# Optimization experiments

Measured on AMD Instinct MI355X. Metric: run time of the kernel, lower is better.

Reference implementation:

```python
import jax, jax.numpy as jnp
import numpy as np

NEG_SLOPE = 0.2  # PyG GATConv default
BN_EPS = 1e-5
NUM_GRAPHS = 128


def _bn(x, g, b, m, v):
    # eval-mode BatchNorm1d with running stats
    return (x - m) * jax.lax.rsqrt(v + BN_EPS) * g + b


def _gat_conv(x, src, dst, mask, W, a_src, a_dst, bias):
    # PyG GATConv: per-head linear, edge logits LeakyReLU(a_src.Wx_j + a_dst.Wx_i),
    # segment-softmax over incoming edges of each dst node, scatter-add messages.
    N = x.shape[0]
    H, C = a_src.shape
    xw = (x @ W).reshape(N, H, C)                       # [N,H,C]
    logit_s = (xw * a_src).sum(-1)                      # [N,H]
    logit_d = (xw * a_dst).sum(-1)                      # [N,H]
    e = jax.nn.leaky_relu(logit_s[src] + logit_d[dst], NEG_SLOPE)  # [E,H]
    e = jnp.where(mask[:, None], e, -1e30)              # edges filtered by edge_weights==1
    m = jax.ops.segment_max(e, dst, num_segments=N)     # [N,H]
    m = jnp.maximum(m, -1e30)                           # guard empty segments
    p = jnp.exp(e - m[dst]) * mask[:, None].astype(e.dtype)
    denom = jax.ops.segment_sum(p, dst, num_segments=N) + 1e-16
    alpha = p / denom[dst]                              # [E,H]
    out = jax.ops.segment_sum(xw[src] * alpha[..., None], dst, num_segments=N)
    return out.reshape(N, H * C) + bias


def setup_inputs() -> dict:
    key = jax.random.key(0)
    ks = jax.random.split(key, 20)
    N, E, F, G, NC = 20000, 320000, 128, NUM_GRAPHS, 10
    E0, E1, H = 256, 512, 2
    C = E1 // H

    def lin(k, fi, fo):
        return jax.random.normal(k, (fi, fo), jnp.float32) / np.float32(np.sqrt(fi))

    def bn(k, n):
        k1, k2, k3, k4 = jax.random.split(k, 4)
        g = 1.0 + 0.1 * jax.random.normal(k1, (n,), jnp.float32)
        b = 0.1 * jax.random.normal(k2, (n,), jnp.float32)
        m = 0.1 * jax.random.normal(k3, (n,), jnp.float32)
        v = 1.0 + 0.5 * jax.random.uniform(k4, (n,), jnp.float32)
        return g, b, m, v

    d = {}
    d['x'] = jax.random.normal(ks[0], (N, F), jnp.float32)
    d['edge_index'] = jax.random.randint(ks[1], (2, E), 0, N, dtype=jnp.int32)
    d['edge_weights'] = jnp.ones((E,), jnp.int32)
    d['batch'] = jnp.sort(jax.random.randint(ks[2], (N,), 0, G, dtype=jnp.int32))
    d['mlp_w1'] = lin(ks[3], F, E0); d['mlp_b1'] = jnp.zeros((E0,), jnp.float32)
    d['bn1_g'], d['bn1_b'], d['bn1_m'], d['bn1_v'] = bn(ks[4], E0)
    d['mlp_w2'] = lin(ks[5], E0, E0); d['mlp_b2'] = jnp.zeros((E0,), jnp.float32)
    d['bn2_g'], d['bn2_b'], d['bn2_m'], d['bn2_v'] = bn(ks[6], E0)
    d['gat0_w'] = lin(ks[7], E0, H * C)
    d['gat0_asrc'] = 0.1 * jax.random.normal(ks[8], (H, C), jnp.float32)
    d['gat0_adst'] = 0.1 * jax.random.normal(ks[9], (H, C), jnp.float32)
    d['gat0_bias'] = jnp.zeros((H * C,), jnp.float32)
    d['gat1_w'] = lin(ks[10], E1, H * C)
    d['gat1_asrc'] = 0.1 * jax.random.normal(ks[11], (H, C), jnp.float32)
    d['gat1_adst'] = 0.1 * jax.random.normal(ks[12], (H, C), jnp.float32)
    d['gat1_bias'] = jnp.zeros((H * C,), jnp.float32)
    d['bn3_g'], d['bn3_b'], d['bn3_m'], d['bn3_v'] = bn(ks[13], E1)
    d['fin_w1'] = lin(ks[14], E1, E1); d['fin_b1'] = jnp.zeros((E1,), jnp.float32)
    d['fin_w2'] = lin(ks[15], E1, NC); d['fin_b2'] = jnp.zeros((NC,), jnp.float32)
    return d


def reference(x, edge_index, edge_weights, batch,
              mlp_w1, mlp_b1, bn1_g, bn1_b, bn1_m, bn1_v,
              mlp_w2, mlp_b2, bn2_g, bn2_b, bn2_m, bn2_v,
              gat0_w, gat0_asrc, gat0_adst, gat0_bias,
              gat1_w, gat1_asrc, gat1_adst, gat1_bias,
              bn3_g, bn3_b, bn3_m, bn3_v,
              fin_w1, fin_b1, fin_w2, fin_b2):
    src, dst = edge_index[0], edge_index[1]
    mask = edge_weights == 1
    # initial MLP (dropout is identity in eval)
    h = jax.nn.relu(_bn(x @ mlp_w1 + mlp_b1, bn1_g, bn1_b, bn1_m, bn1_v))
    h = jax.nn.relu(_bn(h @ mlp_w2 + mlp_b2, bn2_g, bn2_b, bn2_m, bn2_v))
    # GAT layers
    h = _gat_conv(h, src, dst, mask, gat0_w, gat0_asrc, gat0_adst, gat0_bias)
    h = _gat_conv(h, src, dst, mask, gat1_w, gat1_asrc, gat1_adst, gat1_bias)
    # global mean pool over graphs
    sums = jax.ops.segment_sum(h, batch, num_segments=NUM_GRAPHS)
    cnt = jax.ops.segment_sum(jnp.ones((h.shape[0], 1), h.dtype), batch, num_segments=NUM_GRAPHS)
    pooled = sums / jnp.maximum(cnt, 1.0)
    # final head: BN -> ReLU -> Linear -> ReLU -> Linear
    z = jax.nn.relu(_bn(pooled, bn3_g, bn3_b, bn3_m, bn3_v))
    z = jax.nn.relu(z @ fin_w1 + fin_b1)
    return z @ fin_w2 + fin_b2
```

## Files before the change

kernel.cpp:

```cpp
#include <hip/hip_runtime.h>

typedef unsigned short u16;

constexpr int NN = 20000;
constexpr int EE = 320000;
constexpr int FD = 128;
constexpr int C0 = 256;
constexpr int C1 = 512;
constexpr int NG = 128;
constexpr int NC = 10;
constexpr int NBLK = (NN + 255) / 256;
constexpr int HB  = 320;
constexpr int EST = HB * 256;

constexpr size_t OFF_XB   = 0;
constexpr size_t OFF_H1   = OFF_XB  + (size_t)NN * FD * 2;
constexpr size_t OFF_H2   = OFF_H1  + (size_t)NN * C0 * 2;
constexpr size_t OFF_XW   = OFF_H2  + (size_t)NN * C0 * 2;
constexpr size_t OFF_H34  = OFF_XW  + (size_t)NN * C1 * 2;
constexpr size_t OFF_LS   = OFF_H34 + (size_t)NN * C1 * 2;
constexpr size_t OFF_LD   = OFF_LS  + (size_t)NN * 2 * 4;
constexpr size_t OFF_DEG  = OFF_LD  + (size_t)NN * 2 * 4;
constexpr size_t OFF_OFFS = OFF_DEG + (size_t)NN * 4;
constexpr size_t OFF_CUR  = OFF_OFFS + 80016;
constexpr size_t OFF_CSRC = OFF_CUR + (size_t)NN * 4;
constexpr size_t OFF_GCNT = OFF_CSRC + (size_t)EE * 4;
constexpr size_t OFF_GOFF = OFF_GCNT + 512;
constexpr size_t OFF_PART = OFF_GOFF + 768;
constexpr size_t OFF_PTOT = OFF_PART + 512;
constexpr size_t OFF_Z1   = OFF_PTOT + 256;
constexpr size_t OFF_Z2   = OFF_Z1  + (size_t)NG * C1 * 2;
constexpr size_t OFF_ST   = OFF_Z2  + (size_t)NG * C1 * 2;
constexpr size_t OFF_W1T  = OFF_ST  + 8192;
constexpr size_t OFF_W2T  = OFF_W1T + (size_t)FD * C0 * 2;
constexpr size_t OFF_G0T  = OFF_W2T + (size_t)C0 * C0 * 2;
constexpr size_t OFF_G1T  = OFF_G0T + (size_t)C0 * C1 * 2;
constexpr size_t OFF_AUX  = OFF_G1T + (size_t)C1 * C1 * 2;
constexpr size_t OFF_FLAG = OFF_AUX  + 0;
constexpr size_t OFF_A0S  = OFF_AUX  + 256;
constexpr size_t OFF_A0D  = OFF_AUX  + 1280;
constexpr size_t OFF_A1S  = OFF_AUX  + 2304;
constexpr size_t OFF_A1D  = OFF_AUX  + 3328;
constexpr size_t OFF_GB0  = OFF_AUX  + 4352;
constexpr size_t OFF_GB1  = OFF_AUX  + 6400;
constexpr size_t OFF_FB1  = OFF_AUX  + 8448;
constexpr size_t OFF_FB2  = OFF_AUX  + 10496;
constexpr size_t OFF_GMX  = OFF_AUX  + 10752;

__device__ inline float bf2f(u16 u) { return __uint_as_float(((unsigned)u) << 16); }
__device__ inline u16 f2bf(float f) {
    unsigned u = __float_as_uint(f);
    unsigned r = u + 0x7fffu + ((u >> 16) & 1u);
    return (u16)(r >> 16);
}
__device__ inline float ldf(const void* p, long i, unsigned f) {
    return f ? ((const float*)p)[i] : bf2f(((const u16*)p)[i]);
}
__device__ inline unsigned encf(float f) {
    unsigned u = __float_as_uint(f);
    return (u & 0x80000000u) ? ~u : (u | 0x80000000u);
}
__device__ inline float decf(unsigned e) {
    return (e & 0x80000000u) ? __uint_as_float(e ^ 0x80000000u) : __uint_as_float(~e);
}
__device__ inline void unpack8(uint4 r, float* v) {
    v[0] = bf2f((u16)(r.x & 0xffff)); v[1] = bf2f((u16)(r.x >> 16));
    v[2] = bf2f((u16)(r.y & 0xffff)); v[3] = bf2f((u16)(r.y >> 16));
    v[4] = bf2f((u16)(r.z & 0xffff)); v[5] = bf2f((u16)(r.z >> 16));
    v[6] = bf2f((u16)(r.w & 0xffff)); v[7] = bf2f((u16)(r.w >> 16));
}

typedef __bf16 bf16x8_t __attribute__((ext_vector_type(8)));
typedef float  f32x4_t  __attribute__((ext_vector_type(4)));

__device__ __forceinline__ void gl_lds16(const u16* g, u16* l) {
    __builtin_amdgcn_global_load_lds((const __attribute__((address_space(1))) void*)g,
                                     (__attribute__((address_space(3))) void*)l, 16, 0, 0);
}

__global__ void detect_dtype(const u16* __restrict__ x, const u16* __restrict__ w,
                             const u16* __restrict__ fw, unsigned* flag) {
    __shared__ int cnt;
    if (threadIdx.x == 0) cnt = 0;
    __syncthreads();
    int c = 0;
    for (int i = threadIdx.x; i < 4096; i += 256) {
        c += (((x[i]  >> 7) & 0xFF) == 0xFF);
        c += (((w[i]  >> 7) & 0xFF) == 0xFF);
        c += (((fw[i] >> 7) & 0xFF) == 0xFF);
    }
    atomicAdd(&cnt, c);
    __syncthreads();
    if (threadIdx.x == 0) *flag = (cnt >= 2) ? 1u : 0u;
}

__global__ void cvt_x(const unsigned* __restrict__ flag, const void* __restrict__ xin,
                      u16* __restrict__ XB, int* __restrict__ deg, int* __restrict__ gcnt,
                      unsigned* __restrict__ gmxu) {
    int i = blockIdx.x * 256 + threadIdx.x;
    if (i < NN) deg[i] = 0;
    if (i < NG) gcnt[i] = 0;
    if (i < 4)  gmxu[i] = encf(-1e30f);
    if (*flag) {
        float4 v = ((const float4*)xin)[i];
        ushort4 r;
        r.x = f2bf(v.x); r.y = f2bf(v.y); r.z = f2bf(v.z); r.w = f2bf(v.w);
        ((ushort4*)XB)[i] = r;
    } else {
        ((ushort4*)XB)[i] = ((const ushort4*)xin)[i];
    }
}

__global__ void prep_params(const unsigned* __restrict__ flag,
                            const void* g1, const void* b1, const void* m1, const void* v1, const void* lb1,
                            const void* g2, const void* b2, const void* m2, const void* v2, const void* lb2,
                            const void* g3, const void* b3, const void* m3, const void* v3,
                            const void* a0s, const void* a0d, const void* gb0in,
                            const void* a1s, const void* a1d, const void* gb1in,
                            const void* fb1in, const void* fb2in,
                            float* S1, float* T1, float* S2, float* T2, float* S3, float* T3,
                            u16* A0S, u16* A0D, u16* A1S, u16* A1D,
                            float* GB0, float* GB1, float* FB1, float* FB2) {
    unsigned f = *flag;
    int c = threadIdx.x;
    if (c < 256) {
        float s = ldf(g1, c, f) / sqrtf(ldf(v1, c, f) + 1e-5f);
        S1[c] = s; T1[c] = s * (ldf(lb1, c, f) - ldf(m1, c, f)) + ldf(b1, c, f);
        float s2 = ldf(g2, c, f) / sqrtf(ldf(v2, c, f) + 1e-5f);
        S2[c] = s2; T2[c] = s2 * (ldf(lb2, c, f) - ldf(m2, c, f)) + ldf(b2, c, f);
    }
    float s3 = ldf(g3, c, f) / sqrtf(ldf(v3, c, f) + 1e-5f);
    S3[c] = s3; T3[c] = ldf(b3, c, f) - ldf(m3, c, f) * s3;
    A0S[c] = f2bf(ldf(a0s, c, f));
    A0D[c] = f2bf(ldf(a0d, c, f));
    A1S[c] = f2bf(ldf(a1s, c, f));
    A1D[c] = f2bf(ldf(a1d, c, f));
    GB0[c] = ldf(gb0in, c, f);
    GB1[c] = ldf(gb1in, c, f);
    FB1[c] = ldf(fb1in, c, f);
    if (c < NC) FB2[c] = ldf(fb2in, c, f);
}

__global__ void transpose_all(const unsigned* __restrict__ flag,
                              const void* __restrict__ w1, const void* __restrict__ w2,
                              const void* __restrict__ g0, const void* __restrict__ g1,
                              u16* __restrict__ w1T, u16* __restrict__ w2T,
                              u16* __restrict__ g0T, u16* __restrict__ g1T) {
    int b = blockIdx.x;
    const void* B; u16* BT; int K, logN, base;
    if (b < 128)      { B = w1; BT = w1T; K = FD; logN = 8; base = 0; }
    else if (b < 384) { B = w2; BT = w2T; K = C0; logN = 8; base = 128; }
    else if (b < 896) { B = g0; BT = g0T; K = C0; logN = 9; base = 384; }
    else              { B = g1; BT = g1T; K = C1; logN = 9; base = 896; }
    int idx = (b - base) * 256 + threadIdx.x;
    int N = 1 << logN;
    int k = idx >> logN, n = idx & (N - 1);
    u16 v = (*flag) ? f2bf(((const float*)B)[idx]) : ((const u16*)B)[idx];
    BT[(size_t)n * K + k] = v;
}

__global__ __launch_bounds__(256) void hist_k(const int* __restrict__ dst, const int* __restrict__ ew,
                                              const int* __restrict__ batch,
                                              int* __restrict__ deg, int* __restrict__ gcnt) {
    int tid = blockIdx.x * 256 + threadIdx.x;
    int lane = threadIdx.x & 63;
#pragma unroll
    for (int j = 0; j < 4; j++) {
        int e = tid + j * EST;
        if (e < EE && ew[e] == 1) atomicAdd(&deg[dst[e]], 1);
    }
    int n = tid;
    if (n < NN) {
        int g = batch[n];
        int pg = __shfl_up(g, 1);
        bool head = (lane == 0) || (pg != g);
        unsigned long long act = __ballot(1);
        unsigned long long hm  = __ballot(head);
        if (head) {
            unsigned long long above = (lane < 63) ? ((hm >> (lane + 1)) << (lane + 1)) : 0ull;
            int limit = 64 - __builtin_clzll(act);
            int nxt = above ? __builtin_ctzll(above) : limit;
            atomicAdd(&gcnt[g], nxt - lane);
        }
    }
}
__global__ __launch_bounds__(256) void scan_blk(const int* __restrict__ deg, int* __restrict__ off,
                                                int* __restrict__ part) {
    __shared__ int tmp[256];
    int tid = threadIdx.x, i = blockIdx.x * 256 + tid;
    int v = (i < NN) ? deg[i] : 0;
    tmp[tid] = v;
    __syncthreads();
#pragma unroll
    for (int s = 1; s < 256; s <<= 1) {
        int a = (tid >= s) ? tmp[tid - s] : 0;
        __syncthreads();
        if (tid >= s) tmp[tid] += a;
        __syncthreads();
    }
    if (i < NN) off[i] = tmp[tid] - v;
    if (tid == 255) part[blockIdx.x] = tmp[255];
}
__global__ __launch_bounds__(128) void scan_small(int* __restrict__ part, int* __restrict__ ptot,
                                                  const int* __restrict__ gcnt, int* __restrict__ goff) {
    __shared__ int tmp[128];
    int tid = threadIdx.x;
    int v = (tid < NBLK) ? part[tid] : 0;
    tmp[tid] = v;
    __syncthreads();
#pragma unroll
    for (int s = 1; s < 128; s <<= 1) {
        int a = (tid >= s) ? tmp[tid - s] : 0;
        __syncthreads();
        if (tid >= s) tmp[tid] += a;
        __syncthreads();
    }
    if (tid < NBLK) part[tid] = tmp[tid] - v;
    if (tid == 127) *ptot = tmp[127];
    __syncthreads();
    int g = gcnt[tid];
    tmp[tid] = g;
    __syncthreads();
#pragma unroll
    for (int s = 1; s < 128; s <<= 1) {
        int a = (tid >= s) ? tmp[tid - s] : 0;
        __syncthreads();
        if (tid >= s) tmp[tid] += a;
        __syncthreads();
    }
    goff[tid] = tmp[tid] - g;
    if (tid == 127) goff[128] = tmp[127];
}
__global__ __launch_bounds__(256) void scan_add(int* __restrict__ off, const int* __restrict__ part,
                                                const int* __restrict__ ptot, int* __restrict__ cursor) {
    int tid = threadIdx.x, i = blockIdx.x * 256 + tid;
    if (i < NN) {
        int o = off[i] + part[blockIdx.x];
        off[i] = o;
        cursor[i] = o;
    }
    if (i == 0) off[NN] = *ptot;
}
__global__ __launch_bounds__(256) void csr_fill(const int* __restrict__ src, const int* __restrict__ dst,
                                                const int* __restrict__ ew,
                                                int* __restrict__ cursor, int* __restrict__ csrc) {
    int tid = blockIdx.x * 256 + threadIdx.x;
    bool ok[4]; int sv[4]; int p[4];
#pragma unroll
    for (int j = 0; j < 4; j++) {
        int e = tid + j * EST;
        ok[j] = false; sv[j] = 0; p[j] = 0;
        if (e < EE && ew[e] == 1) {
            ok[j] = true;
            sv[j] = src[e];
            p[j] = atomicAdd(&cursor[dst[e]], 1);
        }
    }
#pragma unroll
    for (int j = 0; j < 4; j++) if (ok[j]) csrc[p[j]] = sv[j];
}

template <int EPI>
__global__ __launch_bounds__(256) void gemm_tile(const u16* __restrict__ A, const u16* __restrict__ BT,
                                                 u16* __restrict__ Cm,
                                                 const float* __restrict__ S, const float* __restrict__ T,
                                                 int M, int N, int K) {
    __shared__ u16 As[128 * 32];
    __shared__ u16 Bs[128 * 32];
    const int tid  = threadIdx.x;
    const int wave = tid >> 6;
    const int lane = tid & 63;
    const int quad = lane >> 4;
    const int l16  = lane & 15;
    const int wr0  = (wave >> 1) * 64;
    const int wc0  = (wave & 1) * 64;
    const int row0 = blockIdx.x * 128;
    const int col0 = blockIdx.y * 128;

    const int lr = lane >> 2;
    const int lk = (lane & 3) * 8;
    int r0l = wave * 32 + lr;
    int r1l = r0l + 16;
    int gr0 = row0 + r0l; if (gr0 >= M) gr0 = M - 1;
    int gr1 = row0 + r1l; if (gr1 >= M) gr1 = M - 1;
    const u16* ga0 = A  + (size_t)gr0 * K + lk;
    const u16* ga1 = A  + (size_t)gr1 * K + lk;
    const u16* gb0 = BT + (size_t)(col0 + r0l) * K + lk;
    const u16* gb1 = BT + (size_t)(col0 + r1l) * K + lk;
    u16* la0 = As + (size_t)(wave * 32)      * 32 + lane * 8;
    u16* la1 = As + (size_t)(wave * 32 + 16) * 32 + lane * 8;
    u16* lb0 = Bs + (size_t)(wave * 32)      * 32 + lane * 8;
    u16* lb1 = Bs + (size_t)(wave * 32 + 16) * 32 + lane * 8;

    f32x4_t acc[4][4];
#pragma unroll
    for (int r = 0; r < 4; r++)
#pragma unroll
        for (int c = 0; c < 4; c++)
#pragma unroll
            for (int i = 0; i < 4; i++) acc[r][c][i] = 0.f;

    for (int k0 = 0; k0 < K; k0 += 32) {
        gl_lds16(ga0 + k0, la0);
        gl_lds16(ga1 + k0, la1);
        gl_lds16(gb0 + k0, lb0);
        gl_lds16(gb1 + k0, lb1);
        __syncthreads();

        bf16x8_t a[4], b[4];
#pragma unroll
        for (int r = 0; r < 4; r++)
            a[r] = *(const bf16x8_t*)(As + (size_t)(wr0 + r * 16 + l16) * 32 + quad * 8);
#pragma unroll
        for (int c = 0; c < 4; c++)
            b[c] = *(const bf16x8_t*)(Bs + (size_t)(wc0 + c * 16 + l16) * 32 + quad * 8);
#pragma unroll
        for (int r = 0; r < 4; r++)
#pragma unroll
            for (int c = 0; c < 4; c++)
                acc[r][c] = __builtin_amdgcn_mfma_f32_16x16x32_bf16(a[r], b[c], acc[r][c], 0, 0, 0);
        __syncthreads();
    }

#pragma unroll
    for (int r = 0; r < 4; r++) {
        int rb = row0 + wr0 + r * 16 + quad * 4;
#pragma unroll
        for (int c = 0; c < 4; c++) {
            int col = col0 + wc0 + c * 16 + l16;
            float sc = (EPI == 1) ? S[col] : 0.f;
            float sh = (EPI == 1) ? T[col] : 0.f;
#pragma unroll
            for (int i = 0; i < 4; i++) {
                int row = rb + i;
                if (row < M) {
                    float v = acc[r][c][i];
                    if (EPI == 1) v = fmaxf(v * sc + sh, 0.f);
                    Cm[(size_t)row * N + col] = f2bf(v);
                }
            }
        }
    }
}

__global__ __launch_bounds__(256) void gat_logits(const u16* __restrict__ xw, const u16* __restrict__ asrc,
                                                  const u16* __restrict__ adst, float* __restrict__ ls,
                                                  float* __restrict__ ld) {
    int n = blockIdx.x * 4 + (threadIdx.x >> 6);
    if (n >= NN) return;
    int lane = threadIdx.x & 63;
    uint4 xv = ((const uint4*)(xw + (size_t)n * C1))[lane];
    uint4 sv = ((const uint4*)asrc)[lane];
    uint4 dv = ((const uint4*)adst)[lane];
    float x[8], a[8], d[8];
    unpack8(xv, x); unpack8(sv, a); unpack8(dv, d);
    float ps = 0.f, pd = 0.f;
#pragma unroll
    for (int j = 0; j < 8; j++) { ps += x[j] * a[j]; pd += x[j] * d[j]; }
#pragma unroll
    for (int m = 16; m >= 1; m >>= 1) { ps += __shfl_xor(ps, m); pd += __shfl_xor(pd, m); }
    if ((lane & 31) == 0) {
        int h = lane >> 5;
        ls[n * 2 + h] = ps;
        ld[n * 2 + h] = pd;
    }
}

__global__ __launch_bounds__(256) void ls_max(const float* __restrict__ ls, unsigned* __restrict__ gmx) {
    int tid = blockIdx.x * 256 + threadIdx.x;
    float m0 = -1e30f, m1 = -1e30f;
    for (int n = tid; n < NN; n += 40 * 256) {
        float2 v = ((const float2*)ls)[n];
        m0 = fmaxf(m0, v.x); m1 = fmaxf(m1, v.y);
    }
#pragma unroll
    for (int o = 32; o >= 1; o >>= 1) {
        m0 = fmaxf(m0, __shfl_xor(m0, o));
        m1 = fmaxf(m1, __shfl_xor(m1, o));
    }
    if ((threadIdx.x & 63) == 0) {
        atomicMax(&gmx[0], encf(m0));
        atomicMax(&gmx[1], encf(m1));
    }
}

__global__ __launch_bounds__(256) void gat_aggregate(const int* __restrict__ off, const int* __restrict__ csrc,
                                                     const float* __restrict__ ls, const float* __restrict__ ld,
                                                     const unsigned* __restrict__ gmx, const u16* __restrict__ xw,
                                                     const float* __restrict__ bias, u16* __restrict__ outh) {
    int n = blockIdx.x * 4 + (threadIdx.x >> 6);
    if (n >= NN) return;
    int lane = threadIdx.x & 63;
    int h = lane >> 5;
    int beg = off[n], end = off[n + 1];
    float ldh = ld[n * 2 + h];
    float gm = decf(gmx[h]) + ldh;
    float mhat = gm > 0.f ? gm : 0.2f * gm;

    float acc[8];
#pragma unroll
    for (int j = 0; j < 8; j++) acc[j] = 0.f;
    float den = 0.f;

    float lsv = 0.f; uint4 row;
    if (beg < end) {
        int s0 = csrc[beg];
        lsv = ls[s0 * 2 + h];
        row = ((const uint4*)(xw + (size_t)s0 * C1))[lane];
    }
    for (int i = beg; i < end; i++) {
        float cls = lsv;
        uint4 crow = row;
        if (i + 1 < end) {
            int s2 = csrc[i + 1];
            lsv = ls[s2 * 2 + h];
            row = ((const uint4*)(xw + (size_t)s2 * C1))[lane];
        }
        float v = cls + ldh;
        v = v > 0.f ? v : 0.2f * v;
        float p = __expf(v - mhat);
        den += p;
        float x[8];
        unpack8(crow, x);
#pragma unroll
        for (int j = 0; j < 8; j++) acc[j] = fmaf(p, x[j], acc[j]);
    }

    float inv = 1.f / fmaxf(den, 1e-30f);
    ushort4 r0, r1;
    int cb = lane * 8;
    float o0 = acc[0] * inv + bias[cb + 0], o1 = acc[1] * inv + bias[cb + 1];
    float o2 = acc[2] * inv + bias[cb + 2], o3 = acc[3] * inv + bias[cb + 3];
    float o4 = acc[4] * inv + bias[cb + 4], o5 = acc[5] * inv + bias[cb + 5];
    float o6 = acc[6] * inv + bias[cb + 6], o7 = acc[7] * inv + bias[cb + 7];
    r0.x = f2bf(o0); r0.y = f2bf(o1); r0.z = f2bf(o2); r0.w = f2bf(o3);
    r1.x = f2bf(o4); r1.y = f2bf(o5); r1.z = f2bf(o6); r1.w = f2bf(o7);
    ushort4* dst4 = (ushort4*)(outh + (size_t)n * C1 + cb);
    dst4[0] = r0; dst4[1] = r1;
}

__global__ __launch_bounds__(512) void pool_bn(const u16* __restrict__ h4, const int* __restrict__ goff,
                                               const float* __restrict__ S3, const float* __restrict__ T3,
                                               u16* __restrict__ z1) {
    int g = blockIdx.x, t = threadIdx.x;
    int b = goff[g], e = goff[g + 1];
    float s = 0.f;
    for (int n = b; n < e; n++) s += bf2f(h4[(size_t)n * C1 + t]);
    float mean = s / fmaxf((float)(e - b), 1.f);
    float v = mean * S3[t] + T3[t];
    z1[(size_t)g * C1 + t] = f2bf(fmaxf(v, 0.f));
}

__global__ __launch_bounds__(512) void head_fc1(const unsigned* __restrict__ flag, const u16* __restrict__ z1,
                                                const void* __restrict__ w1, const float* __restrict__ FB1,
                                                u16* __restrict__ z2) {
    __shared__ float zrow[512];
    int g = blockIdx.x, t = threadIdx.x;
    zrow[t] = bf2f(z1[(size_t)g * 512 + t]);
    __syncthreads();
    float acc = 0.f;
    if (*flag) {
        const float* w = (const float*)w1;
        for (int k = 0; k < 512; k++) acc = fmaf(zrow[k], w[(size_t)k * 512 + t], acc);
    } else {
        const u16* w = (const u16*)w1;
        for (int k = 0; k < 512; k++) acc = fmaf(zrow[k], bf2f(w[(size_t)k * 512 + t]), acc);
    }
    acc += FB1[t];
    z2[(size_t)g * 512 + t] = f2bf(fmaxf(acc, 0.f));
}
__global__ __launch_bounds__(64) void head_fc2(const unsigned* __restrict__ flag, const u16* __restrict__ z2,
                                               const void* __restrict__ w2, const float* __restrict__ FB2,
                                               void* __restrict__ out) {
    int g = blockIdx.x, o = blockIdx.y, lane = threadIdx.x;
    unsigned f = *flag;
    float acc = 0.f;
    if (f) {
        const float* w = (const float*)w2;
        for (int k = lane; k < 512; k += 64) acc += bf2f(z2[(size_t)g * 512 + k]) * w[(size_t)k * NC + o];
    } else {
        const u16* w = (const u16*)w2;
        for (int k = lane; k < 512; k += 64) acc += bf2f(z2[(size_t)g * 512 + k]) * bf2f(w[(size_t)k * NC + o]);
    }
#pragma unroll
    for (int m = 32; m >= 1; m >>= 1) acc += __shfl_xor(acc, m);
    if (lane == 0) {
        float v = acc + FB2[o];
        if (f) ((float*)out)[g * NC + o] = v;
        else   ((u16*)out)[g * NC + o] = f2bf(v);
    }
}

extern "C" void kernel_launch(void* const* d_in, const int* in_sizes, int n_in,
                              void* d_out, int out_size, void* d_ws, size_t ws_size,
                              hipStream_t stream) {
    (void)in_sizes; (void)n_in; (void)out_size; (void)ws_size;

    const void* x      = d_in[0];
    const int* ei      = (const int*)d_in[1];
    const int* src     = ei;
    const int* dst     = ei + EE;
    const int* ew      = (const int*)d_in[2];
    const int* batch   = (const int*)d_in[3];
    const void* mlp_w1 = d_in[4];
    const void* mlp_b1 = d_in[5];
    const void *bn1g = d_in[6], *bn1b = d_in[7], *bn1m = d_in[8], *bn1v = d_in[9];
    const void* mlp_w2 = d_in[10];
    const void* mlp_b2 = d_in[11];
    const void *bn2g = d_in[12], *bn2b = d_in[13], *bn2m = d_in[14], *bn2v = d_in[15];
    const void* g0w    = d_in[16];
    const void* g0as   = d_in[17];
    const void* g0ad   = d_in[18];
    const void* g0bias = d_in[19];
    const void* g1w    = d_in[20];
    const void* g1as   = d_in[21];
    const void* g1ad   = d_in[22];
    const void* g1bias = d_in[23];
    const void *bn3g = d_in[24], *bn3b = d_in[25], *bn3m = d_in[26], *bn3v = d_in[27];
    const void* fin_w1 = d_in[28];
    const void* fin_b1 = d_in[29];
    const void* fin_w2 = d_in[30];
    const void* fin_b2 = d_in[31];

    char* ws = (char*)d_ws;
    u16*  XB   = (u16*)(ws + OFF_XB);
    u16*  h1   = (u16*)(ws + OFF_H1);
    u16*  h2   = (u16*)(ws + OFF_H2);
    u16*  xw   = (u16*)(ws + OFF_XW);
    u16*  h34  = (u16*)(ws + OFF_H34);
    float* ls  = (float*)(ws + OFF_LS);
    float* ld  = (float*)(ws + OFF_LD);
    int*  deg  = (int*)(ws + OFF_DEG);
    int*  off  = (int*)(ws + OFF_OFFS);
    int*  cur  = (int*)(ws + OFF_CUR);
    int*  csrc = (int*)(ws + OFF_CSRC);
    int*  gcnt = (int*)(ws + OFF_GCNT);
    int*  goff = (int*)(ws + OFF_GOFF);
    int*  part = (int*)(ws + OFF_PART);
    int*  ptot = (int*)(ws + OFF_PTOT);
    u16*  z1   = (u16*)(ws + OFF_Z1);
    u16*  z2   = (u16*)(ws + OFF_Z2);
    float* S1 = (float*)(ws + OFF_ST);
    float* T1 = S1 + 256;
    float* S2 = T1 + 256;
    float* T2 = S2 + 256;
    float* S3 = T2 + 256;
    float* T3 = S3 + 512;
    u16* w1T = (u16*)(ws + OFF_W1T);
    u16* w2T = (u16*)(ws + OFF_W2T);
    u16* g0T = (u16*)(ws + OFF_G0T);
    u16* g1T = (u16*)(ws + OFF_G1T);
    unsigned* flag = (unsigned*)(ws + OFF_FLAG);
    u16* A0S = (u16*)(ws + OFF_A0S);
    u16* A0D = (u16*)(ws + OFF_A0D);
    u16* A1S = (u16*)(ws + OFF_A1S);
    u16* A1D = (u16*)(ws + OFF_A1D);
    float* GB0 = (float*)(ws + OFF_GB0);
    float* GB1 = (float*)(ws + OFF_GB1);
    float* FB1 = (float*)(ws + OFF_FB1);
    float* FB2 = (float*)(ws + OFF_FB2);
    unsigned* GMXU = (unsigned*)(ws + OFF_GMX);

    detect_dtype<<<1, 256, 0, stream>>>((const u16*)x, (const u16*)mlp_w1, (const u16*)fin_w1, flag);
    cvt_x<<<(NN * FD / 4) / 256, 256, 0, stream>>>(flag, x, XB, deg, gcnt, GMXU);
    prep_params<<<1, 512, 0, stream>>>(flag,
                                       bn1g, bn1b, bn1m, bn1v, mlp_b1,
                                       bn2g, bn2b, bn2m, bn2v, mlp_b2,
                                       bn3g, bn3b, bn3m, bn3v,
                                       g0as, g0ad, g0bias, g1as, g1ad, g1bias,
                                       fin_b1, fin_b2,
                                       S1, T1, S2, T2, S3, T3,
                                       A0S, A0D, A1S, A1D, GB0, GB1, FB1, FB2);
    transpose_all<<<1920, 256, 0, stream>>>(flag, mlp_w1, mlp_w2, g0w, g1w, w1T, w2T, g0T, g1T);

    hist_k<<<HB, 256, 0, stream>>>(dst, ew, batch, deg, gcnt);
    scan_blk<<<NBLK, 256, 0, stream>>>(deg, off, part);
    scan_small<<<1, 128, 0, stream>>>(part, ptot, gcnt, goff);
    scan_add<<<NBLK, 256, 0, stream>>>(off, part, ptot, cur);
    csr_fill<<<HB, 256, 0, stream>>>(src, dst, ew, cur, csrc);

    gemm_tile<1><<<dim3(157, 2), 256, 0, stream>>>(XB, w1T, h1, S1, T1, NN, C0, FD);
    gemm_tile<1><<<dim3(157, 2), 256, 0, stream>>>(h1, w2T, h2, S2, T2, NN, C0, C0);

    gemm_tile<0><<<dim3(157, 4), 256, 0, stream>>>(h2, g0T, xw, nullptr, nullptr, NN, C1, C0);
    gat_logits<<<NN / 4, 256, 0, stream>>>(xw, A0S, A0D, ls, ld);
    ls_max<<<40, 256, 0, stream>>>(ls, GMXU);
    gat_aggregate<<<NN / 4, 256, 0, stream>>>(off, csrc, ls, ld, GMXU, xw, GB0, h34);

    gemm_tile<0><<<dim3(157, 4), 256, 0, stream>>>(h34, g1T, xw, nullptr, nullptr, NN, C1, C1);
    gat_logits<<<NN / 4, 256, 0, stream>>>(xw, A1S, A1D, ls, ld);
    ls_max<<<40, 256, 0, stream>>>(ls, GMXU + 2);
    gat_aggregate<<<NN / 4, 256, 0, stream>>>(off, csrc, ls, ld, GMXU + 2, xw, GB1, h34);

    pool_bn<<<NG, 512, 0, stream>>>(h34, goff, S3, T3, z1);
    head_fc1<<<NG, 512, 0, stream>>>(flag, z1, fin_w1, FB1, z2);
    head_fc2<<<dim3(NG, NC), 64, 0, stream>>>(flag, z2, fin_w2, FB2, d_out);
}
```

Before: 433.9 us.

## Batch GAT edge gathers in double-buffered chunks of eight; fuse max into logits

The aggregation loop now gathers source rows in chunks of eight edges with two register buffers, so many row loads are in flight at once instead of one-ahead prefetch. The separate ls_max kernel is removed and each node's source logit is atomically maxed into the global per-head max inside gat_logits. This targets memory latency in the gather-bound aggregation and saves two launches, at the cost of many more atomics (one per node per head) and higher register pressure, which may lower occupancy.

```diff
diff --git a/kernel.cpp b/kernel.cpp
--- a/kernel.cpp
+++ b/kernel.cpp
@@ -345,7 +345,7 @@
 
 __global__ __launch_bounds__(256) void gat_logits(const u16* __restrict__ xw, const u16* __restrict__ asrc,
                                                   const u16* __restrict__ adst, float* __restrict__ ls,
-                                                  float* __restrict__ ld) {
+                                                  float* __restrict__ ld, unsigned* __restrict__ gmx) {
     int n = blockIdx.x * 4 + (threadIdx.x >> 6);
     if (n >= NN) return;
     int lane = threadIdx.x & 63;
@@ -363,24 +363,7 @@
         int h = lane >> 5;
         ls[n * 2 + h] = ps;
         ld[n * 2 + h] = pd;
-    }
-}
-
-__global__ __launch_bounds__(256) void ls_max(const float* __restrict__ ls, unsigned* __restrict__ gmx) {
-    int tid = blockIdx.x * 256 + threadIdx.x;
-    float m0 = -1e30f, m1 = -1e30f;
-    for (int n = tid; n < NN; n += 40 * 256) {
-        float2 v = ((const float2*)ls)[n];
-        m0 = fmaxf(m0, v.x); m1 = fmaxf(m1, v.y);
-    }
-#pragma unroll
-    for (int o = 32; o >= 1; o >>= 1) {
-        m0 = fmaxf(m0, __shfl_xor(m0, o));
-        m1 = fmaxf(m1, __shfl_xor(m1, o));
-    }
-    if ((threadIdx.x & 63) == 0) {
-        atomicMax(&gmx[0], encf(m0));
-        atomicMax(&gmx[1], encf(m1));
+        atomicMax(&gmx[h], encf(ps));
     }
 }
 
@@ -393,6 +376,7 @@
     int lane = threadIdx.x & 63;
     int h = lane >> 5;
     int beg = off[n], end = off[n + 1];
+    int deg = end - beg;
     float ldh = ld[n * 2 + h];
     float gm = decf(gmx[h]) + ldh;
     float mhat = gm > 0.f ? gm : 0.2f * gm;
@@ -402,28 +386,50 @@
     for (int j = 0; j < 8; j++) acc[j] = 0.f;
     float den = 0.f;
 
-    float lsv = 0.f; uint4 row;
-    if (beg < end) {
-        int s0 = csrc[beg];
-        lsv = ls[s0 * 2 + h];
-        row = ((const uint4*)(xw + (size_t)s0 * C1))[lane];
-    }
-    for (int i = beg; i < end; i++) {
-        float cls = lsv;
-        uint4 crow = row;
-        if (i + 1 < end) {
-            int s2 = csrc[i + 1];
-            lsv = ls[s2 * 2 + h];
-            row = ((const uint4*)(xw + (size_t)s2 * C1))[lane];
+    if (deg > 0) {
+        int nch = (deg + 7) >> 3;
+        int last = end - 1;
+
+        float lsA[8], lsB[8];
+        uint4 rA[8], rB[8];
+
+        auto loadChunk = [&](int ch, float* lsb, uint4* rowb) {
+            int base = beg + ch * 8;
+            int idx[8];
+#pragma unroll
+            for (int j = 0; j < 8; j++) { int e = base + j; idx[j] = csrc[e <= last ? e : last]; }
+#pragma unroll
+            for (int j = 0; j < 8; j++) {
+                lsb[j] = ls[idx[j] * 2 + h];
+                rowb[j] = ((const uint4*)(xw + (size_t)idx[j] * C1))[lane];
+            }
+        };
+        auto procChunk = [&](int ch, const float* lsb, const uint4* rowb) {
+            int base = beg + ch * 8;
+#pragma unroll
+            for (int j = 0; j < 8; j++) {
+                float v = lsb[j] + ldh;
+                v = v > 0.f ? v : 0.2f * v;
+                float p = (base + j < end) ? __expf(v - mhat) : 0.f;
+                den += p;
+                float xv[8];
+                unpack8(rowb[j], xv);
+#pragma unroll
+                for (int q = 0; q < 8; q++) acc[q] = fmaf(p, xv[q], acc[q]);
+            }
+        };
+
+        loadChunk(0, lsA, rA);
+        if (nch > 1) loadChunk(1, lsB, rB);
+        int c = 0;
+        while (true) {
+            procChunk(c, lsA, rA); c++;
+            if (c >= nch) break;
+            if (c + 1 < nch) loadChunk(c + 1, lsA, rA);
+            procChunk(c, lsB, rB); c++;
+            if (c >= nch) break;
+            if (c + 1 < nch) loadChunk(c + 1, lsB, rB);
         }
-        float v = cls + ldh;
-        v = v > 0.f ? v : 0.2f * v;
-        float p = __expf(v - mhat);
-        den += p;
-        float x[8];
-        unpack8(crow, x);
-#pragma unroll
-        for (int j = 0; j < 8; j++) acc[j] = fmaf(p, x[j], acc[j]);
     }
 
     float inv = 1.f / fmaxf(den, 1e-30f);
@@ -583,13 +589,11 @@
     gemm_tile<1><<<dim3(157, 2), 256, 0, stream>>>(h1, w2T, h2, S2, T2, NN, C0, C0);
 
     gemm_tile<0><<<dim3(157, 4), 256, 0, stream>>>(h2, g0T, xw, nullptr, nullptr, NN, C1, C0);
-    gat_logits<<<NN / 4, 256, 0, stream>>>(xw, A0S, A0D, ls, ld);
-    ls_max<<<40, 256, 0, stream>>>(ls, GMXU);
+    gat_logits<<<NN / 4, 256, 0, stream>>>(xw, A0S, A0D, ls, ld, GMXU);
     gat_aggregate<<<NN / 4, 256, 0, stream>>>(off, csrc, ls, ld, GMXU, xw, GB0, h34);
 
     gemm_tile<0><<<dim3(157, 4), 256, 0, stream>>>(h34, g1T, xw, nullptr, nullptr, NN, C1, C1);
-    gat_logits<<<NN / 4, 256, 0, stream>>>(xw, A1S, A1D, ls, ld);
-    ls_max<<<40, 256, 0, stream>>>(ls, GMXU + 2);
+    gat_logits<<<NN / 4, 256, 0, stream>>>(xw, A1S, A1D, ls, ld, GMXU + 2);
     gat_aggregate<<<NN / 4, 256, 0, stream>>>(off, csrc, ls, ld, GMXU + 2, xw, GB1, h34);
 
     pool_bn<<<NG, 512, 0, stream>>>(h34, goff, S3, T3, z1);
```

New measurement: 881.8 us. +103.2%, slower.
